# Optimization experiments

Hardware: AMD Instinct MI355X
Metric: run time of the kernel (lower is better)

## Reference

```python
import jax, jax.numpy as jnp
import numpy as np

D_MODEL = 1024
N_HEADS = 16
D_K = 64
D_V = 64
B = 2
S = 2048


def setup_inputs() -> dict:
    key = jax.random.key(0)
    ks = jax.random.split(key, 7)
    q = jax.random.normal(ks[0], (B, S, D_MODEL), dtype=jnp.float32)
    k = jax.random.normal(ks[1], (B, S, D_MODEL), dtype=jnp.float32)
    v = jax.random.normal(ks[2], (B, S, D_MODEL), dtype=jnp.float32)
    mask = jnp.ones((B, S, S), dtype=bool)
    sc = 1.0 / np.sqrt(D_MODEL)
    Wq = jax.random.normal(ks[3], (D_MODEL, N_HEADS * D_K), dtype=jnp.float32) * sc
    Wk = jax.random.normal(ks[4], (D_MODEL, N_HEADS * D_K), dtype=jnp.float32) * sc
    Wv = jax.random.normal(ks[5], (D_MODEL, N_HEADS * D_V), dtype=jnp.float32) * sc
    Wo = jax.random.normal(ks[6], (N_HEADS * D_V, D_MODEL), dtype=jnp.float32) * sc
    return {"q": q, "k": k, "v": v, "mask": mask,
            "Wq": Wq, "Wk": Wk, "Wv": Wv, "Wo": Wo}


def reference(q, k, v, mask, Wq, Wk, Wv, Wo):
    # projections (no bias)
    qh = (q @ Wq).reshape(B, S, N_HEADS, D_K).transpose(0, 2, 1, 3)  # [B,H,Sq,dk]
    kh = (k @ Wk).reshape(B, S, N_HEADS, D_K).transpose(0, 2, 1, 3)  # [B,H,Sk,dk]
    vh = (v @ Wv).reshape(B, S, N_HEADS, D_V).transpose(0, 2, 1, 3)  # [B,H,Sk,dv]
    # NOTE: original module does NOT scale by 1/sqrt(d_k)
    scores = jnp.einsum('bhqd,bhkd->bhqk', qh, kh)  # [B,H,Sq,Sk]
    scores = jnp.where(mask[:, None, :, :], scores, -jnp.inf)
    attn = jax.nn.softmax(scores, axis=-1)
    # dropout p=0.0 -> identity (eval mode)
    out = jnp.einsum('bhqk,bhkd->bhqd', attn, vh)  # [B,H,Sq,dv]
    out = out.transpose(0, 2, 1, 3).reshape(B, S, N_HEADS * D_V)
    return out @ Wo  # [B,S,d_model]
```

## Files before the change

### kernel.cpp

```cpp
#include <hip/hip_runtime.h>

typedef _Float16 half_t;
typedef _Float16 half8 __attribute__((ext_vector_type(8)));
typedef _Float16 half4 __attribute__((ext_vector_type(4)));
typedef float f32x4 __attribute__((ext_vector_type(4)));
typedef unsigned int uint2v __attribute__((ext_vector_type(2)));
typedef unsigned int uint4v __attribute__((ext_vector_type(4)));
typedef unsigned short ushort4v __attribute__((ext_vector_type(4)));
typedef unsigned short ushort8 __attribute__((ext_vector_type(8)));
typedef __bf16 bf16x8_t __attribute__((ext_vector_type(8)));

#define LOG2E 1.4426950408889634f

#define MFMA32_BF16(A, B, C) __builtin_amdgcn_mfma_f32_16x16x32_bf16((A), (B), (C), 0, 0, 0)

__device__ __forceinline__ void gl2lds16(const void* g, void* l) {
    __builtin_amdgcn_global_load_lds(
        (const __attribute__((address_space(1))) void*)g,
        (__attribute__((address_space(3))) void*)l, 16, 0, 0);
}

__device__ __forceinline__ unsigned cvt_pk_bf16(float a, float b) {
    unsigned r;
    asm("v_cvt_pk_bf16_f32 %0, %1, %2" : "=v"(r) : "v"(a), "v"(b));
    return r;
}

__device__ __forceinline__ unsigned short bf16_bits(float a) {
    return (unsigned short)((__builtin_bit_cast(unsigned, a) + 0x8000u) >> 16);
}

__global__ __launch_bounds__(256) void prep_kernel(
    const float* __restrict__ q, const float* __restrict__ k,
    const float* __restrict__ v,
    const float* __restrict__ W0, const float* __restrict__ W1,
    const float* __restrict__ W2, const float* __restrict__ W3,
    half_t* __restrict__ X, half_t* __restrict__ WqkvT, half_t* __restrict__ WoT)
{
    __shared__ __attribute__((aligned(16))) float T[64][65];
    const int bid = blockIdx.x;
    if (bid < 12288) {
        size_t t = (size_t)bid * 256 + threadIdx.x;
        size_t e = t * 4;
        int id = (int)(e >> 22);
        const float* src = (id == 0) ? q : (id == 1) ? k : v;
        size_t off = e & ((1u << 22) - 1);
        float4 f = *(const float4*)(src + off);
        half4 hv = { (half_t)f.x, (half_t)f.y, (half_t)f.z, (half_t)f.w };
        *(half4*)(X + e) = hv;
        return;
    }
    const int bid2 = bid - 12288;
    const int z = bid2 >> 8;
    const int y = (bid2 >> 4) & 15;
    const int x = bid2 & 15;
    const float* W = (z == 0) ? W0 : (z == 1) ? W1 : (z == 2) ? W2 : W3;
    half_t* D = (z == 0) ? WqkvT : (z == 1) ? WqkvT + 1048576
              : (z == 2) ? WqkvT + 2097152 : WoT;
    const float sc = (z == 0) ? LOG2E : 1.0f;
    const int r0 = y * 64;
    const int c0 = x * 64;
    const int tid = threadIdx.x;
    const int tr = tid >> 4;
    const int tc = (tid & 15) * 4;
#pragma unroll
    for (int p = 0; p < 4; ++p) {
        int r = p * 16 + tr;
        float4 f = *(const float4*)(W + (size_t)(r0 + r) * 1024 + c0 + tc);
        T[r][tc + 0] = f.x; T[r][tc + 1] = f.y; T[r][tc + 2] = f.z; T[r][tc + 3] = f.w;
    }
    __syncthreads();
#pragma unroll
    for (int p = 0; p < 4; ++p) {
        int n = p * 16 + tr;
        half4 hv = { (half_t)(T[tc + 0][n] * sc), (half_t)(T[tc + 1][n] * sc),
                     (half_t)(T[tc + 2][n] * sc), (half_t)(T[tc + 3][n] * sc) };
        *(half4*)(D + (size_t)(c0 + n) * 1024 + r0 + tc) = hv;
    }
}

__global__ __launch_bounds__(256) void gemm_qkv_kernel(
    const half_t* __restrict__ A,
    const half_t* __restrict__ Bt0, const half_t* __restrict__ Bt1,
    const half_t* __restrict__ Bt2,
    half_t* __restrict__ C, unsigned short* __restrict__ VhtOut)
{
    __shared__ __attribute__((aligned(16))) char smem[32768];
    const int tid = threadIdx.x;
    const int lane = tid & 63;
    const int w = tid >> 6;
    const int quad = lane >> 4;
    const int l16 = lane & 15;
    const int wm = w >> 1, wn = w & 1;
    const int swz4 = l16 & 3;
    const int N = 1024;

    const int m0 = blockIdx.x * 128;
    const int n0 = blockIdx.y * 128;
    const int slab = blockIdx.x >> 5;
    const half_t* Bt = (slab == 0) ? Bt0 : (slab == 1) ? Bt1 : Bt2;

    int cA0 = tid, cA1 = tid + 256;
    const half_t* gA0 = A + (size_t)(m0 + (cA0 >> 2)) * 1024 + (((cA0 & 3) ^ ((cA0 >> 2) & 3)) * 8);
    const half_t* gA1 = A + (size_t)(m0 + (cA1 >> 2)) * 1024 + (((cA1 & 3) ^ ((cA1 >> 2) & 3)) * 8);
    const half_t* gB0 = Bt + (size_t)(n0 + (cA0 >> 2)) * 1024 + (((cA0 & 3) ^ ((cA0 >> 2) & 3)) * 8);
    const half_t* gB1 = Bt + (size_t)(n0 + (cA1 >> 2)) * 1024 + (((cA1 & 3) ^ ((cA1 >> 2) & 3)) * 8);
    const int lA0 = tid * 16, lA1 = (tid + 256) * 16;
    const int lB0 = 8192 + tid * 16, lB1 = 8192 + (tid + 256) * 16;

    f32x4 acc[4][4] = {};

    gl2lds16(gA0, smem + lA0); gl2lds16(gA1, smem + lA1);
    gl2lds16(gB0, smem + lB0); gl2lds16(gB1, smem + lB1);
    gA0 += 32; gA1 += 32; gB0 += 32; gB1 += 32;

    for (int kt = 0; kt < 32; ++kt) {
        __syncthreads();
        const int cur = (kt & 1) * 16384;
        if (kt < 31) {
            const int nxt = 16384 - cur;
            gl2lds16(gA0, smem + nxt + lA0); gl2lds16(gA1, smem + nxt + lA1);
            gl2lds16(gB0, smem + nxt + lB0); gl2lds16(gB1, smem + nxt + lB1);
            gA0 += 32; gA1 += 32; gB0 += 32; gB1 += 32;
        }
        const half_t* As = (const half_t*)(smem + cur);
        const half_t* Bs = (const half_t*)(smem + cur + 8192);
        half8 af[4], bf[4];
#pragma unroll
        for (int mt = 0; mt < 4; ++mt)
            af[mt] = *(const half8*)&As[(wm * 64 + mt * 16 + l16) * 32 + ((quad ^ swz4) * 8)];
#pragma unroll
        for (int nt = 0; nt < 4; ++nt)
            bf[nt] = *(const half8*)&Bs[(wn * 64 + nt * 16 + l16) * 32 + ((quad ^ swz4) * 8)];
#pragma unroll
        for (int mt = 0; mt < 4; ++mt)
#pragma unroll
            for (int nt = 0; nt < 4; ++nt)
                acc[mt][nt] = __builtin_amdgcn_mfma_f32_16x16x32_f16(
                    af[mt], bf[nt], acc[mt][nt], 0, 0, 0);
    }

    if (slab < 2) {
#pragma unroll
        for (int mt = 0; mt < 4; ++mt) {
            int rbase = m0 + wm * 64 + mt * 16 + quad * 4;
#pragma unroll
            for (int nt = 0; nt < 4; ++nt) {
                int col = n0 + wn * 64 + nt * 16 + l16;
#pragma unroll
                for (int r = 0; r < 4; ++r)
                    C[(size_t)(rbase + r) * N + col] = (half_t)acc[mt][nt][r];
            }
        }
    } else {
        unsigned short* Tr = (unsigned short*)smem;
        const int tok0 = m0 - 8192;
        const int bb = tok0 >> 11;
        const int ss0 = tok0 & 2047;
#pragma unroll
        for (int p = 0; p < 2; ++p) {
            __syncthreads();
#pragma unroll
            for (int t16 = 0; t16 < 2; ++t16) {
                int nt = 2 * p + t16;
                int c = wn * 32 + t16 * 16 + l16;
#pragma unroll
                for (int mt = 0; mt < 4; ++mt) {
                    int sb = wm * 64 + mt * 16 + quad * 4;
                    ushort4v pk = { bf16_bits(acc[mt][nt][0]), bf16_bits(acc[mt][nt][1]),
                                    bf16_bits(acc[mt][nt][2]), bf16_bits(acc[mt][nt][3]) };
                    *(ushort4v*)&Tr[c * 136 + sb] = pk;
                }
            }
            __syncthreads();
            int cc = tid >> 2, seg = tid & 3;
            int colit = ((cc >> 5) << 6) + 32 * p + (cc & 31);
            int ncol = n0 + colit;
            int row_out = ((bb << 4) + (ncol >> 6)) * 64 + (ncol & 63);
            unsigned short* gdst = VhtOut + (size_t)row_out * 2048 + ss0 + seg * 32;
            const unsigned short* lsrc = Tr + cc * 136 + seg * 32;
#pragma unroll
            for (int u = 0; u < 4; ++u) {
                ushort4v lo = *(const ushort4v*)(lsrc + u * 4);
                ushort4v hi = *(const ushort4v*)(lsrc + u * 4 + 16);
                ushort8 o = { lo[0], lo[1], lo[2], lo[3], hi[0], hi[1], hi[2], hi[3] };
                *(ushort8*)(gdst + u * 8) = o;
            }
        }
    }
}

__global__ __launch_bounds__(256) void gemm_bt_m64_kernel(
    const half_t* __restrict__ A, const half_t* __restrict__ Bt,
    float* __restrict__ C)
{
    __shared__ __attribute__((aligned(16))) char smem[24576];
    const int tid = threadIdx.x;
    const int lane = tid & 63;
    const int w = tid >> 6;
    const int quad = lane >> 4;
    const int l16 = lane & 15;
    const int wm = w >> 1, wn = w & 1;
    const int swz4 = l16 & 3;
    const int N = 1024;

    const int m0 = blockIdx.x * 64;
    const int n0 = blockIdx.y * 128;

    int c0 = tid, c1 = tid + 256;
    const half_t* gA0 = A + (size_t)(m0 + (c0 >> 2)) * 1024 + (((c0 & 3) ^ ((c0 >> 2) & 3)) * 8);
    const half_t* gB0 = Bt + (size_t)(n0 + (c0 >> 2)) * 1024 + (((c0 & 3) ^ ((c0 >> 2) & 3)) * 8);
    const half_t* gB1 = Bt + (size_t)(n0 + (c1 >> 2)) * 1024 + (((c1 & 3) ^ ((c1 >> 2) & 3)) * 8);
    const int lA0 = tid * 16;
    const int lB0 = 4096 + tid * 16, lB1 = 4096 + (tid + 256) * 16;

    f32x4 acc[2][4] = {};

    gl2lds16(gA0, smem + lA0);
    gl2lds16(gB0, smem + lB0); gl2lds16(gB1, smem + lB1);
    gA0 += 32; gB0 += 32; gB1 += 32;

    for (int kt = 0; kt < 32; ++kt) {
        __syncthreads();
        const int cur = (kt & 1) * 12288;
        if (kt < 31) {
            const int nxt = 12288 - cur;
            gl2lds16(gA0, smem + nxt + lA0);
            gl2lds16(gB0, smem + nxt + lB0); gl2lds16(gB1, smem + nxt + lB1);
            gA0 += 32; gB0 += 32; gB1 += 32;
        }
        const half_t* As = (const half_t*)(smem + cur);
        const half_t* Bs = (const half_t*)(smem + cur + 4096);
        half8 af[2], bf[4];
#pragma unroll
        for (int mt = 0; mt < 2; ++mt)
            af[mt] = *(const half8*)&As[(wm * 32 + mt * 16 + l16) * 32 + ((quad ^ swz4) * 8)];
#pragma unroll
        for (int nt = 0; nt < 4; ++nt)
            bf[nt] = *(const half8*)&Bs[(wn * 64 + nt * 16 + l16) * 32 + ((quad ^ swz4) * 8)];
#pragma unroll
        for (int mt = 0; mt < 2; ++mt)
#pragma unroll
            for (int nt = 0; nt < 4; ++nt)
                acc[mt][nt] = __builtin_amdgcn_mfma_f32_16x16x32_f16(
                    af[mt], bf[nt], acc[mt][nt], 0, 0, 0);
    }
#pragma unroll
    for (int mt = 0; mt < 2; ++mt) {
        int rbase = m0 + wm * 32 + mt * 16 + quad * 4;
#pragma unroll
        for (int nt = 0; nt < 4; ++nt) {
            int col = n0 + wn * 64 + nt * 16 + l16;
#pragma unroll
            for (int r = 0; r < 4; ++r)
                C[(size_t)(rbase + r) * N + col] = acc[mt][nt][r];
        }
    }
}

__global__ __launch_bounds__(512, 4) void attn_kernel(
    const half_t* __restrict__ Qh, const half_t* __restrict__ Kh,
    const unsigned short* __restrict__ Vht, half_t* __restrict__ Out)
{
    __shared__ __attribute__((aligned(16))) char smem[65536];

    const int tid = threadIdx.x;
    const int lane = tid & 63;
    const int w = tid >> 6;
    const int wq = w & 3;
    const int ws = w >> 2;
    const int quad = lane >> 4;
    const int l16 = lane & 15;
    const int swz = l16 & 7;

    const int bid = blockIdx.x;
    const int bh = bid & 31;
    const int qt = bid >> 5;
    const int h = bh & 15;
    const int b = bh >> 4;
    const int qrow0 = b * 2048 + qt * 128;
    const int qbase = qrow0 + wq * 32;

    half8 qf[2][2];
#pragma unroll
    for (int qg = 0; qg < 2; ++qg)
#pragma unroll
        for (int ks = 0; ks < 2; ++ks)
            qf[qg][ks] = *(const half8*)(Qh + (size_t)(qbase + qg * 16 + l16) * 1024
                                         + h * 64 + ks * 32 + quad * 8);

    const half_t* kp[2]; const unsigned short* vp[2];
    int ldk[2], ldv[2];
#pragma unroll
    for (int i = 0; i < 2; ++i) {
        int c = i * 512 + tid;
        int rK = c >> 3, gK = (c & 7) ^ (rK & 7);
        kp[i] = Kh + (size_t)(b * 2048 + rK) * 1024 + h * 64 + gK * 8;
        ldk[i] = c * 16;
        int rV = c >> 4, gV = (c & 15) ^ (rV & 7);
        vp[i] = Vht + (size_t)(bh * 64 + rV) * 2048 + gV * 8;
        ldv[i] = 16384 + c * 16;
    }

    f32x4 accT[2][4] = {};
    f32x4 accL[2] = {};
    const ushort8 onesu = { 0x3F80, 0x3F80, 0x3F80, 0x3F80,
                            0x3F80, 0x3F80, 0x3F80, 0x3F80 };
    const bf16x8_t ones8 = __builtin_bit_cast(bf16x8_t, onesu);

#pragma unroll
    for (int i = 0; i < 2; ++i) {
        gl2lds16(kp[i], (char*)smem + ldk[i]);
        gl2lds16(vp[i], (char*)smem + ldv[i]);
        kp[i] += 128 * 1024; vp[i] += 128;
    }

    for (int kt = 0; kt < 16; ++kt) {
        __syncthreads();
        const int cur = (kt & 1) * 32768;
        if (kt < 15) {
            const int nxt = 32768 - cur;
#pragma unroll
            for (int i = 0; i < 2; ++i) {
                gl2lds16(kp[i], (char*)smem + nxt + ldk[i]);
                gl2lds16(vp[i], (char*)smem + nxt + ldv[i]);
                kp[i] += 128 * 1024; vp[i] += 128;
            }
        }
        const half_t* Ksp = (const half_t*)(smem + cur);
        const unsigned short* Vsp = (const unsigned short*)(smem + cur + 16384);

        uint4v pbu[2][2];
#pragma unroll
        for (int t = 0; t < 4; ++t) {
            int srow = ws * 64 + t * 16 + l16;
            half8 k0 = *(const half8*)&Ksp[srow * 64 + ((quad ^ swz) * 8)];
            half8 k1 = *(const half8*)&Ksp[srow * 64 + (((4 + quad) ^ swz) * 8)];
#pragma unroll
            for (int qg = 0; qg < 2; ++qg) {
                f32x4 z = {};
                z = __builtin_amdgcn_mfma_f32_16x16x32_f16(k0, qf[qg][0], z, 0, 0, 0);
                z = __builtin_amdgcn_mfma_f32_16x16x32_f16(k1, qf[qg][1], z, 0, 0, 0);
                float e0 = __builtin_amdgcn_exp2f(z[0]);
                float e1 = __builtin_amdgcn_exp2f(z[1]);
                float e2 = __builtin_amdgcn_exp2f(z[2]);
                float e3 = __builtin_amdgcn_exp2f(z[3]);
                pbu[qg][t >> 1][(t & 1) * 2 + 0] = cvt_pk_bf16(e0, e1);
                pbu[qg][t >> 1][(t & 1) * 2 + 1] = cvt_pk_bf16(e2, e3);
            }
        }

        __builtin_amdgcn_s_setprio(1);
#pragma unroll
        for (int t2 = 0; t2 < 2; ++t2) {
            bf16x8_t p0 = __builtin_bit_cast(bf16x8_t, pbu[0][t2]);
            bf16x8_t p1 = __builtin_bit_cast(bf16x8_t, pbu[1][t2]);
#pragma unroll
            for (int dt = 0; dt < 4; ++dt) {
                int row = dt * 16 + l16;
                uint4v vv = *(const uint4v*)&Vsp[row * 128 + ((((ws * 2 + t2) * 4 + quad) ^ swz) << 3)];
                bf16x8_t vf = __builtin_bit_cast(bf16x8_t, vv);
                accT[0][dt] = MFMA32_BF16(vf, p0, accT[0][dt]);
                accT[1][dt] = MFMA32_BF16(vf, p1, accT[1][dt]);
            }
            accL[0] = MFMA32_BF16(ones8, p0, accL[0]);
            accL[1] = MFMA32_BF16(ones8, p1, accL[1]);
        }
        __builtin_amdgcn_s_setprio(0);
    }

    __syncthreads();
    float* RB = (float*)smem;
    float* RL = (float*)(smem + 32768);
    if (w >= 4) {
        int wb = w - 4;
#pragma unroll
        for (int qg = 0; qg < 2; ++qg) {
#pragma unroll
            for (int dt = 0; dt < 4; ++dt)
                *(f32x4*)&RB[(((wb * 2 + qg) * 4 + dt) << 8) + lane * 4] = accT[qg][dt];
            RL[((wb * 2 + qg) << 6) + lane] = accL[qg][0];
        }
    }
    __syncthreads();
    float sum0 = 0.0f, sum1 = 0.0f;
    if (w < 4) {
#pragma unroll
        for (int qg = 0; qg < 2; ++qg)
#pragma unroll
            for (int dt = 0; dt < 4; ++dt)
                accT[qg][dt] += *(const f32x4*)&RB[(((w * 2 + qg) * 4 + dt) << 8) + lane * 4];
        sum0 = accL[0][0] + RL[((w * 2 + 0) << 6) + lane];
        sum1 = accL[1][0] + RL[((w * 2 + 1) << 6) + lane];
    }
    __syncthreads();

    if (w < 4) {
        float inv0 = 1.0f / sum0;
        float inv1 = 1.0f / sum1;
        half_t* Ob = (half_t*)smem + w * (32 * 72);
#pragma unroll
        for (int qg = 0; qg < 2; ++qg) {
            float iv = qg ? inv1 : inv0;
#pragma unroll
            for (int dt = 0; dt < 4; ++dt) {
                f32x4 a = accT[qg][dt];
                half4 hv = { (half_t)(a[0] * iv), (half_t)(a[1] * iv),
                             (half_t)(a[2] * iv), (half_t)(a[3] * iv) };
                *(half4*)&Ob[(qg * 16 + l16) * 72 + dt * 16 + quad * 4] = hv;
            }
        }
    }
    __syncthreads();
    if (w < 4) {
        half_t* Ob = (half_t*)smem + w * (32 * 72);
#pragma unroll
        for (int p = 0; p < 4; ++p) {
            int cid = p * 64 + lane;
            int row = cid >> 3, ch = cid & 7;
            half8 vv = *(const half8*)&Ob[row * 72 + ch * 8];
            *(half8*)(Out + (size_t)(qbase + row) * 1024 + h * 64 + ch * 8) = vv;
        }
    }
}

extern "C" void kernel_launch(void* const* d_in, const int* in_sizes, int n_in,
                              void* d_out, int out_size, void* d_ws, size_t ws_size,
                              hipStream_t stream)
{
    const float* q  = (const float*)d_in[0];
    const float* k  = (const float*)d_in[1];
    const float* v  = (const float*)d_in[2];
    const float* Wq = (const float*)d_in[4];
    const float* Wk = (const float*)d_in[5];
    const float* Wv = (const float*)d_in[6];
    const float* Wo = (const float*)d_in[7];
    float* out = (float*)d_out;
    char* ws = (char*)d_ws;

    half_t* Xqkv    = (half_t*)(ws);
    half_t* AttnOut = (half_t*)(ws + 8388608);
    half_t* WqkvT   = (half_t*)(ws + 25165824);
    half_t* WoT     = (half_t*)(ws + 31457280);
    half_t* QKVh    = (half_t*)(ws + 33554432);
    unsigned short* Vht = (unsigned short*)(QKVh + (size_t)8192 * 1024);

    prep_kernel<<<13312, 256, 0, stream>>>(
        q, k, v, Wq, Wk, Wv, Wo, Xqkv, WqkvT, WoT);
    gemm_qkv_kernel<<<dim3(96, 8), 256, 0, stream>>>(
        Xqkv, WqkvT, WqkvT + 1024 * 1024, WqkvT + 2 * 1024 * 1024,
        QKVh, Vht);
    attn_kernel<<<512, 512, 0, stream>>>(
        QKVh, QKVh + (size_t)4096 * 1024, Vht, AttnOut);
    gemm_bt_m64_kernel<<<dim3(64, 8), 256, 0, stream>>>(
        AttnOut, WoT, out);
}
```

Measured before the change: 227.8 us.

## Enlarge QKV GEMM tiles to 256x256 with deeper K-step and split-phase pipeline

The QKV projection GEMM moves from 128x128 tiles with 256 threads to 256x256 tiles with 512 threads, a 64-wide K step, and 128KB of double-buffered LDS. Each iteration splits into two MFMA half-phases, and the next stage's global-to-LDS loads are issued between them using explicit vmcnt/lgkmcnt waits and barriers. A wider XOR swizzle is used, and the V transpose epilogue is reworked so each wave group writes in turn. The aim is higher arithmetic intensity and better overlap of loads with MFMA. The cost is a grid of only 192 blocks, which under-fills the GPU's compute units, plus high register and LDS pressure.

```diff
diff --git a/kernel.cpp b/kernel.cpp
--- a/kernel.cpp
+++ b/kernel.cpp
@@ -79,71 +79,109 @@
     }
 }
 
-__global__ __launch_bounds__(256) void gemm_qkv_kernel(
+#define QKV_FRAG(P, row, lc) (*(const half8*)&(P)[(row) * 64 + ((((lc) ^ ((row) & 7))) * 8)])
+#define QKV_STAGE(t, d)                                                        \
+    do {                                                                       \
+        _Pragma("unroll")                                                      \
+        for (int i_ = 0; i_ < 4; ++i_) {                                       \
+            gl2lds16(gA[i_] + (t) * 64, smem + (d) * 65536 + ldsA[i_]);        \
+            gl2lds16(gB[i_] + (t) * 64, smem + (d) * 65536 + ldsB[i_]);        \
+        }                                                                      \
+    } while (0)
+
+__global__ __launch_bounds__(512, 2) void gemm_qkv_kernel(
     const half_t* __restrict__ A,
     const half_t* __restrict__ Bt0, const half_t* __restrict__ Bt1,
     const half_t* __restrict__ Bt2,
     half_t* __restrict__ C, unsigned short* __restrict__ VhtOut)
 {
-    __shared__ __attribute__((aligned(16))) char smem[32768];
+    __shared__ __attribute__((aligned(16))) char smem[131072];
     const int tid = threadIdx.x;
     const int lane = tid & 63;
     const int w = tid >> 6;
+    const int wm = w >> 2;
+    const int wn = w & 3;
     const int quad = lane >> 4;
     const int l16 = lane & 15;
-    const int wm = w >> 1, wn = w & 1;
-    const int swz4 = l16 & 3;
     const int N = 1024;
 
-    const int m0 = blockIdx.x * 128;
-    const int n0 = blockIdx.y * 128;
-    const int slab = blockIdx.x >> 5;
+    const int mt0 = blockIdx.x;
+    const int m0 = mt0 * 256;
+    const int n0 = blockIdx.y * 256;
+    const int slab = mt0 >> 4;
     const half_t* Bt = (slab == 0) ? Bt0 : (slab == 1) ? Bt1 : Bt2;
 
-    int cA0 = tid, cA1 = tid + 256;
-    const half_t* gA0 = A + (size_t)(m0 + (cA0 >> 2)) * 1024 + (((cA0 & 3) ^ ((cA0 >> 2) & 3)) * 8);
-    const half_t* gA1 = A + (size_t)(m0 + (cA1 >> 2)) * 1024 + (((cA1 & 3) ^ ((cA1 >> 2) & 3)) * 8);
-    const half_t* gB0 = Bt + (size_t)(n0 + (cA0 >> 2)) * 1024 + (((cA0 & 3) ^ ((cA0 >> 2) & 3)) * 8);
-    const half_t* gB1 = Bt + (size_t)(n0 + (cA1 >> 2)) * 1024 + (((cA1 & 3) ^ ((cA1 >> 2) & 3)) * 8);
-    const int lA0 = tid * 16, lA1 = (tid + 256) * 16;
-    const int lB0 = 8192 + tid * 16, lB1 = 8192 + (tid + 256) * 16;
-
-    f32x4 acc[4][4] = {};
-
-    gl2lds16(gA0, smem + lA0); gl2lds16(gA1, smem + lA1);
-    gl2lds16(gB0, smem + lB0); gl2lds16(gB1, smem + lB1);
-    gA0 += 32; gA1 += 32; gB0 += 32; gB1 += 32;
-
-    for (int kt = 0; kt < 32; ++kt) {
-        __syncthreads();
-        const int cur = (kt & 1) * 16384;
-        if (kt < 31) {
-            const int nxt = 16384 - cur;
-            gl2lds16(gA0, smem + nxt + lA0); gl2lds16(gA1, smem + nxt + lA1);
-            gl2lds16(gB0, smem + nxt + lB0); gl2lds16(gB1, smem + nxt + lB1);
-            gA0 += 32; gA1 += 32; gB0 += 32; gB1 += 32;
-        }
-        const half_t* As = (const half_t*)(smem + cur);
-        const half_t* Bs = (const half_t*)(smem + cur + 8192);
-        half8 af[4], bf[4];
-#pragma unroll
-        for (int mt = 0; mt < 4; ++mt)
-            af[mt] = *(const half8*)&As[(wm * 64 + mt * 16 + l16) * 32 + ((quad ^ swz4) * 8)];
+    const half_t* gA[4]; const half_t* gB[4];
+    int ldsA[4], ldsB[4];
+#pragma unroll
+    for (int i = 0; i < 4; ++i) {
+        int s = i * 512 + tid;
+        int row = s >> 3, pc = s & 7, gc = pc ^ (row & 7);
+        gA[i] = A + (size_t)(m0 + row) * 1024 + gc * 8;
+        ldsA[i] = s * 16;
+        gB[i] = Bt + (size_t)(n0 + row) * 1024 + gc * 8;
+        ldsB[i] = 32768 + s * 16;
+    }
+
+    f32x4 acc[8][4] = {};
+
+    QKV_STAGE(0, 0);
+    QKV_STAGE(1, 1);
+    asm volatile("s_waitcnt vmcnt(8)" ::: "memory");
+    __builtin_amdgcn_sched_barrier(0);
+    __builtin_amdgcn_s_barrier();
+
+    for (int kt = 0; kt < 16; ++kt) {
+        const int cur = kt & 1;
+        const half_t* As = (const half_t*)(smem + cur * 65536);
+        const half_t* Bs = (const half_t*)(smem + cur * 65536 + 32768);
+
+        half8 a0[8], b0[4], a1[8], b1[4];
+#pragma unroll
+        for (int mt = 0; mt < 8; ++mt)
+            a0[mt] = QKV_FRAG(As, wm * 128 + mt * 16 + l16, quad);
 #pragma unroll
         for (int nt = 0; nt < 4; ++nt)
-            bf[nt] = *(const half8*)&Bs[(wn * 64 + nt * 16 + l16) * 32 + ((quad ^ swz4) * 8)];
-#pragma unroll
-        for (int mt = 0; mt < 4; ++mt)
+            b0[nt] = QKV_FRAG(Bs, wn * 64 + nt * 16 + l16, quad);
+#pragma unroll
+        for (int mt = 0; mt < 8; ++mt)
 #pragma unroll
             for (int nt = 0; nt < 4; ++nt)
                 acc[mt][nt] = __builtin_amdgcn_mfma_f32_16x16x32_f16(
-                    af[mt], bf[nt], acc[mt][nt], 0, 0, 0);
+                    a0[mt], b0[nt], acc[mt][nt], 0, 0, 0);
+#pragma unroll
+        for (int mt = 0; mt < 8; ++mt)
+            a1[mt] = QKV_FRAG(As, wm * 128 + mt * 16 + l16, 4 + quad);
+#pragma unroll
+        for (int nt = 0; nt < 4; ++nt)
+            b1[nt] = QKV_FRAG(Bs, wn * 64 + nt * 16 + l16, 4 + quad);
+
+        asm volatile("s_waitcnt lgkmcnt(0)" ::: "memory");
+        __builtin_amdgcn_sched_barrier(0);
+        __builtin_amdgcn_s_barrier();
+
+        if (kt < 14) QKV_STAGE(kt + 2, cur);
+
+#pragma unroll
+        for (int mt = 0; mt < 8; ++mt)
+#pragma unroll
+            for (int nt = 0; nt < 4; ++nt)
+                acc[mt][nt] = __builtin_amdgcn_mfma_f32_16x16x32_f16(
+                    a1[mt], b1[nt], acc[mt][nt], 0, 0, 0);
+
+        if (kt < 14) {
+            asm volatile("s_waitcnt vmcnt(8)" ::: "memory");
+        } else {
+            asm volatile("s_waitcnt vmcnt(0)" ::: "memory");
+        }
+        __builtin_amdgcn_sched_barrier(0);
+        __builtin_amdgcn_s_barrier();
     }
 
     if (slab < 2) {
 #pragma unroll
-        for (int mt = 0; mt < 4; ++mt) {
-            int rbase = m0 + wm * 64 + mt * 16 + quad * 4;
+        for (int mt = 0; mt < 8; ++mt) {
+            int rbase = m0 + wm * 128 + mt * 16 + quad * 4;
 #pragma unroll
             for (int nt = 0; nt < 4; ++nt) {
                 int col = n0 + wn * 64 + nt * 16 + l16;
@@ -158,27 +196,26 @@
         const int bb = tok0 >> 11;
         const int ss0 = tok0 & 2047;
 #pragma unroll
-        for (int p = 0; p < 2; ++p) {
+        for (int g = 0; g < 4; ++g) {
             __syncthreads();
-#pragma unroll
-            for (int t16 = 0; t16 < 2; ++t16) {
-                int nt = 2 * p + t16;
-                int c = wn * 32 + t16 * 16 + l16;
-#pragma unroll
-                for (int mt = 0; mt < 4; ++mt) {
-                    int sb = wm * 64 + mt * 16 + quad * 4;
-                    ushort4v pk = { bf16_bits(acc[mt][nt][0]), bf16_bits(acc[mt][nt][1]),
-                                    bf16_bits(acc[mt][nt][2]), bf16_bits(acc[mt][nt][3]) };
-                    *(ushort4v*)&Tr[c * 136 + sb] = pk;
+            if (wn == g) {
+#pragma unroll
+                for (int mt = 0; mt < 8; ++mt) {
+                    int tokb = wm * 128 + mt * 16 + quad * 4;
+#pragma unroll
+                    for (int nt = 0; nt < 4; ++nt) {
+                        int c = nt * 16 + l16;
+                        ushort4v pk = { bf16_bits(acc[mt][nt][0]), bf16_bits(acc[mt][nt][1]),
+                                        bf16_bits(acc[mt][nt][2]), bf16_bits(acc[mt][nt][3]) };
+                        *(ushort4v*)&Tr[c * 264 + tokb] = pk;
+                    }
                 }
             }
             __syncthreads();
-            int cc = tid >> 2, seg = tid & 3;
-            int colit = ((cc >> 5) << 6) + 32 * p + (cc & 31);
-            int ncol = n0 + colit;
-            int row_out = ((bb << 4) + (ncol >> 6)) * 64 + (ncol & 63);
-            unsigned short* gdst = VhtOut + (size_t)row_out * 2048 + ss0 + seg * 32;
-            const unsigned short* lsrc = Tr + cc * 136 + seg * 32;
+            int c = tid >> 3, ch = tid & 7;
+            const unsigned short* lsrc = Tr + c * 264 + ch * 32;
+            int row_out = ((bb << 4) + (n0 >> 6) + g) * 64 + c;
+            unsigned short* gdst = VhtOut + (size_t)row_out * 2048 + ss0 + ch * 32;
 #pragma unroll
             for (int u = 0; u < 4; ++u) {
                 ushort4v lo = *(const ushort4v*)(lsrc + u * 4);
@@ -447,7 +484,7 @@
 
     prep_kernel<<<13312, 256, 0, stream>>>(
         q, k, v, Wq, Wk, Wv, Wo, Xqkv, WqkvT, WoT);
-    gemm_qkv_kernel<<<dim3(96, 8), 256, 0, stream>>>(
+    gemm_qkv_kernel<<<dim3(48, 4), 512, 0, stream>>>(
         Xqkv, WqkvT, WqkvT + 1024 * 1024, WqkvT + 2 * 1024 * 1024,
         QKVh, Vht);
     attn_kernel<<<512, 512, 0, stream>>>(
```

New measurement: 224.0 us. No clear change (-1.7%).
